# Kernel tuning notes

Measured on AMD Instinct MI355X. Metric: run time of the kernel, lower is better.

## Reference

```python
import jax, jax.numpy as jnp
import numpy as np

B, N, IN_DIM, OUT_DIM = 8, 2048, 256, 256
EDGE_P = 0.02   # adjacency density
MASK_P = 0.9    # fraction of valid nodes


def setup_inputs() -> dict:
    key = jax.random.key(0)
    ks = jax.random.split(key, 8)
    x = jax.random.normal(ks[0], (B, N, IN_DIM), dtype=jnp.float32)
    adj = (jax.random.uniform(ks[1], (B, N, N)) < EDGE_P).astype(jnp.float32)
    mask = (jax.random.uniform(ks[2], (B, N)) < MASK_P).astype(jnp.float32)
    # nn.Linear(in_dim, out_dim): W [out, in], b [out]
    lim1 = 1.0 / np.sqrt(IN_DIM)
    W = jax.random.uniform(ks[3], (OUT_DIM, IN_DIM), minval=-lim1, maxval=lim1, dtype=jnp.float32)
    b = jax.random.uniform(ks[4], (OUT_DIM,), minval=-lim1, maxval=lim1, dtype=jnp.float32)
    # nn.Linear(2*out_dim, 1): weight [1, 2D] split into a1 (acts on h_i), a2 (acts on h_j)
    lim2 = 1.0 / np.sqrt(2 * OUT_DIM)
    a1 = jax.random.uniform(ks[5], (OUT_DIM,), minval=-lim2, maxval=lim2, dtype=jnp.float32)
    a2 = jax.random.uniform(ks[6], (OUT_DIM,), minval=-lim2, maxval=lim2, dtype=jnp.float32)
    att_b = jax.random.uniform(ks[7], (), minval=-lim2, maxval=lim2, dtype=jnp.float32)
    return {"x": x, "adj": adj, "mask": mask, "W": W, "b": b, "a1": a1, "a2": a2, "att_b": att_b}


def reference(x, adj, mask, W, b, a1, a2, att_b):
    # h = Linear(x): [B, N, D]
    h = jnp.einsum('bni,di->bnd', x, W) + b
    # attention(cat([h_i, h_j])) == h_i @ a1 + h_j @ a2 + att_b (linear in each half)
    s1 = h @ a1  # [B, N] -> contributes along i
    s2 = h @ a2  # [B, N] -> contributes along j
    logits = s1[:, :, None] + s2[:, None, :] + att_b  # [B, N, N]
    att = jax.nn.sigmoid(logits) * adj
    att = att * mask[:, :, None] * mask[:, None, :]
    att = att / (jnp.sum(att, axis=-1, keepdims=True) + 1e-8)
    h_new = jnp.einsum('bij,bjd->bid', att, h)
    return h_new * mask[:, :, None]
```

## Files before the change

kernel.cpp:

```cpp
#include <hip/hip_runtime.h>
#include <hip/hip_bf16.h>

#define BB 8
#define NN 2048
#define DD 256
#define MM (BB * NN)

typedef __attribute__((ext_vector_type(8))) short bf16x8_t;
typedef __attribute__((ext_vector_type(4))) float f32x4_t;

__global__ __launch_bounds__(256) void gemm_h(
    const float* __restrict__ x,
    const float* __restrict__ Wt,
    const float* __restrict__ bias,
    __hip_bfloat16* __restrict__ h)
{
    __shared__ __hip_bfloat16 As[64][72];
    __shared__ __hip_bfloat16 Bs[64][72];

    const int tid  = threadIdx.x;
    const int r    = tid >> 2;
    const int cs   = (tid & 3) * 16;
    const int w    = tid >> 6;
    const int lane = tid & 63;
    const int m16  = lane & 15;
    const int quad = lane >> 4;
    const long rowBase = (long)blockIdx.x * 64;
    const int  colBase = blockIdx.y * 64;

    f32x4_t acc[4];
#pragma unroll
    for (int c = 0; c < 4; c++) acc[c] = (f32x4_t){0.f, 0.f, 0.f, 0.f};

    for (int k0 = 0; k0 < 256; k0 += 64) {
        const float4* ag = (const float4*)(x  + (rowBase + r) * 256 + k0 + cs);
        const float4* bg = (const float4*)(Wt + (long)(colBase + r) * 256 + k0 + cs);
        float4 av[4], bv[4];
#pragma unroll
        for (int q = 0; q < 4; q++) { av[q] = ag[q]; bv[q] = bg[q]; }

        __align__(16) __hip_bfloat16 ta[16], tb[16];
#pragma unroll
        for (int q = 0; q < 4; q++) {
            ta[q * 4 + 0] = __float2bfloat16(av[q].x);
            ta[q * 4 + 1] = __float2bfloat16(av[q].y);
            ta[q * 4 + 2] = __float2bfloat16(av[q].z);
            ta[q * 4 + 3] = __float2bfloat16(av[q].w);
            tb[q * 4 + 0] = __float2bfloat16(bv[q].x);
            tb[q * 4 + 1] = __float2bfloat16(bv[q].y);
            tb[q * 4 + 2] = __float2bfloat16(bv[q].z);
            tb[q * 4 + 3] = __float2bfloat16(bv[q].w);
        }

        __syncthreads();
        *(uint4*)&As[r][cs]     = *(uint4*)&ta[0];
        *(uint4*)&As[r][cs + 8] = *(uint4*)&ta[8];
        *(uint4*)&Bs[r][cs]     = *(uint4*)&tb[0];
        *(uint4*)&Bs[r][cs + 8] = *(uint4*)&tb[8];
        __syncthreads();

#pragma unroll
        for (int kk = 0; kk < 64; kk += 32) {
            bf16x8_t af = *(const bf16x8_t*)&As[w * 16 + m16][kk + quad * 8];
#pragma unroll
            for (int c = 0; c < 4; c++) {
                bf16x8_t bf = *(const bf16x8_t*)&Bs[c * 16 + m16][kk + quad * 8];
                acc[c] = __builtin_amdgcn_mfma_f32_16x16x32_bf16(af, bf, acc[c], 0, 0, 0);
            }
        }
    }

#pragma unroll
    for (int c = 0; c < 4; c++) {
        const int col = colBase + c * 16 + m16;
        const float bv = bias[col];
#pragma unroll
        for (int reg = 0; reg < 4; reg++) {
            const long row = rowBase + w * 16 + quad * 4 + reg;
            h[row * 256 + col] = __float2bfloat16(acc[c][reg] + bv);
        }
    }
}

struct __attribute__((aligned(8))) bf4 { __hip_bfloat16 v[4]; };

__global__ __launch_bounds__(256) void s_kernel(
    const __hip_bfloat16* __restrict__ h,
    const float* __restrict__ a1,
    const float* __restrict__ a2,
    const float* __restrict__ mask,
    const float* __restrict__ attb_p,
    float* __restrict__ s1b, float* __restrict__ t2)
{
    const int w = threadIdx.x >> 6;
    const int lane = threadIdx.x & 63;
    const long row = (long)blockIdx.x * 4 + w;

    bf4 hv = *(const bf4*)(h + row * 256 + lane * 4);
    float4 A1 = *(const float4*)(a1 + lane * 4);
    float4 A2 = *(const float4*)(a2 + lane * 4);
    const float h0 = __bfloat162float(hv.v[0]), h1 = __bfloat162float(hv.v[1]);
    const float h2 = __bfloat162float(hv.v[2]), h3 = __bfloat162float(hv.v[3]);
    float p1 = h0 * A1.x + h1 * A1.y + h2 * A1.z + h3 * A1.w;
    float p2 = h0 * A2.x + h1 * A2.y + h2 * A2.z + h3 * A2.w;
#pragma unroll
    for (int off = 32; off; off >>= 1) {
        p1 += __shfl_down(p1, off);
        p2 += __shfl_down(p2, off);
    }
    if (lane == 0) {
        s1b[row] = p1 + attb_p[0];
        t2[row]  = (mask[row] != 0.f) ? p2 : -1e30f;
    }
}

__global__ __launch_bounds__(256) void attn_agg(
    const float* __restrict__ adj,
    const float* __restrict__ mask,
    const __hip_bfloat16* __restrict__ h,
    const float* __restrict__ s1b,
    const float* __restrict__ t2,
    float* __restrict__ out)
{
    __shared__ float2 s_list[1024];
    __shared__ int    s_cnt;
    __shared__ float  s_red[4];
    __shared__ float  s_inv;
    __shared__ float2 s_part[128];

    const int tid = threadIdx.x;
    const int b   = blockIdx.x & 7;
    const int i   = blockIdx.x >> 3;
    const long row   = (long)b * NN + i;
    const long mbase = (long)b * NN;

    const float mask_i = mask[row];
    if (mask_i == 0.f) {
        out[row * 256 + tid] = 0.f;
        return;
    }
    if (tid == 0) s_cnt = 0;
    __syncthreads();

    const float si = s1b[row];
    const float4* arow = (const float4*)(adj + row * NN);
    const float4* trow = (const float4*)(t2 + mbase);

    float4 A0 = arow[tid], A1 = arow[256 + tid];
    float4 T0 = trow[tid], T1 = trow[256 + tid];

    float lsum = 0.f;
#pragma unroll
    for (int g = 0; g < 2; g++) {
        const int jb = g * 1024 + tid * 4;
        const float av[4] = {g ? A1.x : A0.x, g ? A1.y : A0.y, g ? A1.z : A0.z, g ? A1.w : A0.w};
        const float tv[4] = {g ? T1.x : T0.x, g ? T1.y : T0.y, g ? T1.z : T0.z, g ? T1.w : T0.w};
#pragma unroll
        for (int e = 0; e < 4; e++) {
            const float z   = si + tv[e];
            const float sig = __builtin_amdgcn_rcpf(1.f + __expf(-z));
            const float wgt = av[e] * sig;
            lsum += wgt;
            if (wgt != 0.f) {
                const int pos = atomicAdd(&s_cnt, 1);
                if (pos < 1024)
                    s_list[pos] = make_float2(__int_as_float((jb + e) << 9), wgt);
            }
        }
    }

#pragma unroll
    for (int off = 32; off; off >>= 1) lsum += __shfl_down(lsum, off);
    const int lane = tid & 63, wv = tid >> 6;
    if (lane == 0) s_red[wv] = lsum;
    __syncthreads();
    if (tid == 0)
        s_inv = 1.f / (s_red[0] + s_red[1] + s_red[2] + s_red[3] + 1e-8f);
    __syncthreads();

    const int cnt  = min(s_cnt, 1024);
    const float inv = s_inv * mask_i;
    const char* hb = (const char*)(h + mbase * 256);
    const int g  = tid >> 7;
    const int t  = tid & 127;
    const int t4 = t * 4;
    const int half = (cnt + 1) >> 1;
    int k       = g ? half : 0;
    const int end = g ? cnt : half;

    float accx = 0.f, accy = 0.f;
    for (; k + 8 <= end; k += 8) {
        float2 e[8];
#pragma unroll
        for (int q = 0; q < 8; q++) e[q] = s_list[k + q];
        unsigned u[8];
#pragma unroll
        for (int q = 0; q < 8; q++)
            u[q] = *(const unsigned*)(hb + (__float_as_int(e[q].x) + t4));
#pragma unroll
        for (int q = 0; q < 8; q++) {
            accx += e[q].y * __uint_as_float(u[q] << 16);
            accy += e[q].y * __uint_as_float(u[q] & 0xffff0000u);
        }
    }
    for (; k + 4 <= end; k += 4) {
        float2 e[4];
#pragma unroll
        for (int q = 0; q < 4; q++) e[q] = s_list[k + q];
        unsigned u[4];
#pragma unroll
        for (int q = 0; q < 4; q++)
            u[q] = *(const unsigned*)(hb + (__float_as_int(e[q].x) + t4));
#pragma unroll
        for (int q = 0; q < 4; q++) {
            accx += e[q].y * __uint_as_float(u[q] << 16);
            accy += e[q].y * __uint_as_float(u[q] & 0xffff0000u);
        }
    }
    for (; k < end; k++) {
        float2 ee = s_list[k];
        unsigned u = *(const unsigned*)(hb + (__float_as_int(ee.x) + t4));
        accx += ee.y * __uint_as_float(u << 16);
        accy += ee.y * __uint_as_float(u & 0xffff0000u);
    }

    if (g) s_part[t] = make_float2(accx, accy);
    __syncthreads();
    if (!g) {
        const float2 p = s_part[t];
        ((float2*)(out + row * 256))[t] =
            make_float2((accx + p.x) * inv, (accy + p.y) * inv);
    }
}

extern "C" void kernel_launch(void* const* d_in, const int* in_sizes, int n_in,
                              void* d_out, int out_size, void* d_ws, size_t ws_size,
                              hipStream_t stream) {
    const float* x    = (const float*)d_in[0];
    const float* adj  = (const float*)d_in[1];
    const float* mask = (const float*)d_in[2];
    const float* W    = (const float*)d_in[3];
    const float* bias = (const float*)d_in[4];
    const float* a1   = (const float*)d_in[5];
    const float* a2   = (const float*)d_in[6];
    const float* attb = (const float*)d_in[7];
    float* out = (float*)d_out;

    __hip_bfloat16* h = (__hip_bfloat16*)d_ws;
    float* s1b = (float*)((char*)d_ws + (size_t)MM * DD * 2);
    float* t2  = s1b + MM;

    gemm_h<<<dim3(MM / 64, DD / 64), 256, 0, stream>>>(x, W, bias, h);
    s_kernel<<<MM / 4, 256, 0, stream>>>(h, a1, a2, mask, attb, s1b, t2);
    attn_agg<<<MM, 256, 0, stream>>>(adj, mask, h, s1b, t2, out);
}
```

Before: 240.3 us.

## Fuse score projections into GEMM epilogue with full-width column tiles

The GEMM now computes all 256 output columns per block using 512 threads, so each row of h is complete within one block. The s1/s2 attention-score dot products are computed in the epilogue with shuffle and shared-memory reductions, which removes the separate s_kernel launch and its re-read of h. Global loads for the next k-slice are also register-prefetched while the MFMAs run. In exchange there are fewer blocks (256), more shared memory for the larger B tile, and more registers per thread.

```diff
diff --git a/kernel.cpp b/kernel.cpp
--- a/kernel.cpp
+++ b/kernel.cpp
@@ -9,43 +9,61 @@
 typedef __attribute__((ext_vector_type(8))) short bf16x8_t;
 typedef __attribute__((ext_vector_type(4))) float f32x4_t;
 
-__global__ __launch_bounds__(256) void gemm_h(
+__global__ __launch_bounds__(512) void gemm_hs(
     const float* __restrict__ x,
     const float* __restrict__ Wt,
     const float* __restrict__ bias,
-    __hip_bfloat16* __restrict__ h)
+    const float* __restrict__ a1,
+    const float* __restrict__ a2,
+    const float* __restrict__ mask,
+    const float* __restrict__ attb_p,
+    __hip_bfloat16* __restrict__ h,
+    float* __restrict__ s1b,
+    float* __restrict__ t2)
 {
     __shared__ __hip_bfloat16 As[64][72];
-    __shared__ __hip_bfloat16 Bs[64][72];
+    __shared__ __hip_bfloat16 Bs[256][72];
+    __shared__ float s_p1[64], s_p2[64];
 
     const int tid  = threadIdx.x;
-    const int r    = tid >> 2;
-    const int cs   = (tid & 3) * 16;
     const int w    = tid >> 6;
     const int lane = tid & 63;
     const int m16  = lane & 15;
     const int quad = lane >> 4;
+    const int rg   = w & 3;
+    const int cg   = w >> 2;
     const long rowBase = (long)blockIdx.x * 64;
-    const int  colBase = blockIdx.y * 64;
-
-    f32x4_t acc[4];
-#pragma unroll
-    for (int c = 0; c < 4; c++) acc[c] = (f32x4_t){0.f, 0.f, 0.f, 0.f};
+
+    const int ar = tid >> 3;
+    const int ac = (tid & 7) * 8;
+    const int br = tid >> 1;
+    const int bc = (tid & 1) * 32;
+
+    f32x4_t acc[8];
+#pragma unroll
+    for (int c = 0; c < 8; c++) acc[c] = (f32x4_t){0.f, 0.f, 0.f, 0.f};
+
+    float4 av[2], bv[8];
+    {
+        const float4* ag = (const float4*)(x + (rowBase + ar) * 256 + ac);
+        av[0] = ag[0]; av[1] = ag[1];
+        const float4* bg = (const float4*)(Wt + (long)br * 256 + bc);
+#pragma unroll
+        for (int q = 0; q < 8; q++) bv[q] = bg[q];
+    }
 
     for (int k0 = 0; k0 < 256; k0 += 64) {
-        const float4* ag = (const float4*)(x  + (rowBase + r) * 256 + k0 + cs);
-        const float4* bg = (const float4*)(Wt + (long)(colBase + r) * 256 + k0 + cs);
-        float4 av[4], bv[4];
-#pragma unroll
-        for (int q = 0; q < 4; q++) { av[q] = ag[q]; bv[q] = bg[q]; }
-
-        __align__(16) __hip_bfloat16 ta[16], tb[16];
-#pragma unroll
-        for (int q = 0; q < 4; q++) {
+        __align__(16) __hip_bfloat16 ta[8];
+        __align__(16) __hip_bfloat16 tb[32];
+#pragma unroll
+        for (int q = 0; q < 2; q++) {
             ta[q * 4 + 0] = __float2bfloat16(av[q].x);
             ta[q * 4 + 1] = __float2bfloat16(av[q].y);
             ta[q * 4 + 2] = __float2bfloat16(av[q].z);
             ta[q * 4 + 3] = __float2bfloat16(av[q].w);
+        }
+#pragma unroll
+        for (int q = 0; q < 8; q++) {
             tb[q * 4 + 0] = __float2bfloat16(bv[q].x);
             tb[q * 4 + 1] = __float2bfloat16(bv[q].y);
             tb[q * 4 + 2] = __float2bfloat16(bv[q].z);
@@ -53,64 +71,78 @@
         }
 
         __syncthreads();
-        *(uint4*)&As[r][cs]     = *(uint4*)&ta[0];
-        *(uint4*)&As[r][cs + 8] = *(uint4*)&ta[8];
-        *(uint4*)&Bs[r][cs]     = *(uint4*)&tb[0];
-        *(uint4*)&Bs[r][cs + 8] = *(uint4*)&tb[8];
+        *(uint4*)&As[ar][ac] = *(uint4*)&ta[0];
+#pragma unroll
+        for (int q = 0; q < 4; q++)
+            *(uint4*)&Bs[br][bc + q * 8] = *(uint4*)&tb[q * 8];
         __syncthreads();
 
+        if (k0 < 192) {
+            const int kn = k0 + 64;
+            const float4* ag = (const float4*)(x + (rowBase + ar) * 256 + kn + ac);
+            av[0] = ag[0]; av[1] = ag[1];
+            const float4* bg = (const float4*)(Wt + (long)br * 256 + kn + bc);
+#pragma unroll
+            for (int q = 0; q < 8; q++) bv[q] = bg[q];
+        }
+
 #pragma unroll
         for (int kk = 0; kk < 64; kk += 32) {
-            bf16x8_t af = *(const bf16x8_t*)&As[w * 16 + m16][kk + quad * 8];
-#pragma unroll
-            for (int c = 0; c < 4; c++) {
-                bf16x8_t bf = *(const bf16x8_t*)&Bs[c * 16 + m16][kk + quad * 8];
+            bf16x8_t af = *(const bf16x8_t*)&As[rg * 16 + m16][kk + quad * 8];
+#pragma unroll
+            for (int c = 0; c < 8; c++) {
+                bf16x8_t bf = *(const bf16x8_t*)&Bs[cg * 128 + c * 16 + m16][kk + quad * 8];
                 acc[c] = __builtin_amdgcn_mfma_f32_16x16x32_bf16(af, bf, acc[c], 0, 0, 0);
             }
         }
     }
 
-#pragma unroll
-    for (int c = 0; c < 4; c++) {
+    const int colBase = cg * 128;
+    float p1[4] = {0.f, 0.f, 0.f, 0.f};
+    float p2[4] = {0.f, 0.f, 0.f, 0.f};
+    const long rw0 = rowBase + rg * 16 + quad * 4;
+#pragma unroll
+    for (int c = 0; c < 8; c++) {
         const int col = colBase + c * 16 + m16;
-        const float bv = bias[col];
-#pragma unroll
-        for (int reg = 0; reg < 4; reg++) {
-            const long row = rowBase + w * 16 + quad * 4 + reg;
-            h[row * 256 + col] = __float2bfloat16(acc[c][reg] + bv);
-        }
-    }
-}
-
-struct __attribute__((aligned(8))) bf4 { __hip_bfloat16 v[4]; };
-
-__global__ __launch_bounds__(256) void s_kernel(
-    const __hip_bfloat16* __restrict__ h,
-    const float* __restrict__ a1,
-    const float* __restrict__ a2,
-    const float* __restrict__ mask,
-    const float* __restrict__ attb_p,
-    float* __restrict__ s1b, float* __restrict__ t2)
-{
-    const int w = threadIdx.x >> 6;
-    const int lane = threadIdx.x & 63;
-    const long row = (long)blockIdx.x * 4 + w;
-
-    bf4 hv = *(const bf4*)(h + row * 256 + lane * 4);
-    float4 A1 = *(const float4*)(a1 + lane * 4);
-    float4 A2 = *(const float4*)(a2 + lane * 4);
-    const float h0 = __bfloat162float(hv.v[0]), h1 = __bfloat162float(hv.v[1]);
-    const float h2 = __bfloat162float(hv.v[2]), h3 = __bfloat162float(hv.v[3]);
-    float p1 = h0 * A1.x + h1 * A1.y + h2 * A1.z + h3 * A1.w;
-    float p2 = h0 * A2.x + h1 * A2.y + h2 * A2.z + h3 * A2.w;
-#pragma unroll
-    for (int off = 32; off; off >>= 1) {
-        p1 += __shfl_down(p1, off);
-        p2 += __shfl_down(p2, off);
-    }
-    if (lane == 0) {
-        s1b[row] = p1 + attb_p[0];
-        t2[row]  = (mask[row] != 0.f) ? p2 : -1e30f;
+        const float bval = bias[col];
+        const float va1  = a1[col];
+        const float va2  = a2[col];
+#pragma unroll
+        for (int reg = 0; reg < 4; reg++) {
+            const __hip_bfloat16 hv = __float2bfloat16(acc[c][reg] + bval);
+            h[(rw0 + reg) * 256 + col] = hv;
+            const float hr = __bfloat162float(hv);
+            p1[reg] += hr * va1;
+            p2[reg] += hr * va2;
+        }
+    }
+#pragma unroll
+    for (int off = 1; off < 16; off <<= 1) {
+#pragma unroll
+        for (int reg = 0; reg < 4; reg++) {
+            p1[reg] += __shfl_xor(p1[reg], off);
+            p2[reg] += __shfl_xor(p2[reg], off);
+        }
+    }
+    if (cg == 1 && m16 == 0) {
+#pragma unroll
+        for (int reg = 0; reg < 4; reg++) {
+            s_p1[rg * 16 + quad * 4 + reg] = p1[reg];
+            s_p2[rg * 16 + quad * 4 + reg] = p2[reg];
+        }
+    }
+    __syncthreads();
+    if (cg == 0 && m16 == 0) {
+        const float ab = attb_p[0];
+#pragma unroll
+        for (int reg = 0; reg < 4; reg++) {
+            const int rl = rg * 16 + quad * 4 + reg;
+            const long row = rowBase + rl;
+            const float sp1 = p1[reg] + s_p1[rl];
+            const float sp2 = p2[reg] + s_p2[rl];
+            s1b[row] = sp1 + ab;
+            t2[row]  = (mask[row] != 0.f) ? sp2 : -1e30f;
+        }
     }
 }
 
@@ -250,7 +282,6 @@
     float* s1b = (float*)((char*)d_ws + (size_t)MM * DD * 2);
     float* t2  = s1b + MM;
 
-    gemm_h<<<dim3(MM / 64, DD / 64), 256, 0, stream>>>(x, W, bias, h);
-    s_kernel<<<MM / 4, 256, 0, stream>>>(h, a1, a2, mask, attb, s1b, t2);
+    gemm_hs<<<MM / 64, 512, 0, stream>>>(x, W, bias, a1, a2, mask, attb, h, s1b, t2);
     attn_agg<<<MM, 256, 0, stream>>>(adj, mask, h, s1b, t2, out);
 }
```

Result: no change. 238.4 us (-0.8%).
